# Performance work log

Hardware: AMD Instinct MI355X
Metric: run time of the kernel (lower is better)

## Reference

```python
import jax, jax.numpy as jnp
import numpy as np

B, S, D, H, E, K = 4, 2048, 512, 2048, 8, 2


def setup_inputs() -> dict:
    key = jax.random.key(0)
    k0, k1, k2, k3 = jax.random.split(key, 4)
    return {
        "x": jax.random.normal(k0, (B, S, D), jnp.float32),
        "router_w": jax.random.normal(k1, (E, D), jnp.float32) * 0.02,
        "router_b": jnp.zeros((E,), jnp.float32),
        "w1": jax.random.normal(k2, (E, D, H), jnp.float32) * 0.02,
        "b1": jnp.zeros((E, H), jnp.float32),
        "w2": jax.random.normal(k3, (E, H, D), jnp.float32) * 0.02,
        "b2": jnp.zeros((E, D), jnp.float32),
        "top_k": K,
    }


def reference(x, router_w, router_b, w1, b1, w2, b2, top_k):
    # x: [B, S, D]; eval mode (no router noise, no dropout)
    Bb, Ss, Dd = x.shape
    Ee = w1.shape[0]
    xf = x.reshape(-1, Dd)                                   # [T, D], T = B*S
    router_logits = xf @ router_w.T + router_b               # [T, E]
    top_v, top_i = jax.lax.top_k(router_logits, top_k)       # [T, K]
    rw = jax.nn.softmax(top_v, axis=-1)                      # [T, K]
    # combine[t, e] = sum_k rw[t, k] * (top_i[t, k] == e); zero for unrouted experts
    combine = jnp.sum(jax.nn.one_hot(top_i, Ee, dtype=xf.dtype) * rw[..., None], axis=1)  # [T, E]
    out = jnp.zeros_like(xf)
    for e in range(Ee):  # fixed small expert count; each iter is a dense GEMM pair
        h = jax.nn.gelu(xf @ w1[e] + b1[e], approximate=False)  # exact erf GELU like torch nn.GELU
        y = h @ w2[e] + b2[e]                                   # [T, D]
        out = out + combine[:, e:e + 1] * y
    return out.reshape(Bb, Ss, Dd), router_logits
```

## Files before the change

kernel.cpp:

```cpp
#include <hip/hip_runtime.h>
#include <hip/hip_bf16.h>

#define TTOK 8192
#define DDIM 512
#define HDIM 2048
#define NEXP 8
#define RBLK 256
#define RTOK (TTOK / RBLK)

typedef __bf16 bf16x8 __attribute__((ext_vector_type(8)));
typedef float f32x4 __attribute__((ext_vector_type(4)));
typedef unsigned short us8 __attribute__((ext_vector_type(8)));

__device__ __forceinline__ unsigned short f2bf(float f) {
  unsigned int u = __builtin_bit_cast(unsigned int, f);
  u += 0x7fffu + ((u >> 16) & 1u);
  return (unsigned short)(u >> 16);
}

__device__ __forceinline__ void gll16(const void* g, void* l) {
  __builtin_amdgcn_global_load_lds(
      (__attribute__((address_space(1))) void*)g,
      (__attribute__((address_space(3))) void*)l, 16, 0, 0);
}

__global__ __launch_bounds__(256) void k_router(
    const float* __restrict__ x, const float* __restrict__ rw,
    const float* __restrict__ rb, float* __restrict__ logits,
    unsigned short* __restrict__ xb,
    short* __restrict__ texp, unsigned short* __restrict__ tpos,
    float* __restrict__ tgate, int* __restrict__ blockcnt) {
  __shared__ int lcnt[NEXP];
  const int tid = threadIdx.x, wid = tid >> 6, lane = tid & 63;
  if (tid < NEXP) lcnt[tid] = 0;
  __syncthreads();
  float4 w0[NEXP], w1[NEXP];
  float rbv[NEXP];
#pragma unroll
  for (int e = 0; e < NEXP; ++e) {
    const float4* wp = (const float4*)(rw + e * DDIM);
    w0[e] = wp[lane * 2];
    w1[e] = wp[lane * 2 + 1];
    rbv[e] = rb[e];
  }
  const int tbase = blockIdx.x * RTOK;
  for (int it = 0; it < RTOK / 4; ++it) {
    const int t = tbase + it * 4 + wid;
    const float4* xr = (const float4*)(x + (size_t)t * DDIM);
    float4 v0 = xr[lane * 2], v1 = xr[lane * 2 + 1];
    us8 o;
    o[0] = f2bf(v0.x); o[1] = f2bf(v0.y); o[2] = f2bf(v0.z); o[3] = f2bf(v0.w);
    o[4] = f2bf(v1.x); o[5] = f2bf(v1.y); o[6] = f2bf(v1.z); o[7] = f2bf(v1.w);
    *(us8*)(xb + (size_t)t * DDIM + lane * 8) = o;
    float a[NEXP];
#pragma unroll
    for (int e = 0; e < NEXP; ++e)
      a[e] = v0.x * w0[e].x + v0.y * w0[e].y + v0.z * w0[e].z + v0.w * w0[e].w +
             v1.x * w1[e].x + v1.y * w1[e].y + v1.z * w1[e].z + v1.w * w1[e].w;
#pragma unroll
    for (int off = 32; off > 0; off >>= 1)
#pragma unroll
      for (int e = 0; e < NEXP; ++e) a[e] += __shfl_xor(a[e], off, 64);
    if (lane == 0) {
      float lg[NEXP];
#pragma unroll
      for (int e = 0; e < NEXP; ++e) lg[e] = a[e] + rbv[e];
      float4 s0, s1;
      s0.x = lg[0]; s0.y = lg[1]; s0.z = lg[2]; s0.w = lg[3];
      s1.x = lg[4]; s1.y = lg[5]; s1.z = lg[6]; s1.w = lg[7];
      ((float4*)(logits + t * NEXP))[0] = s0;
      ((float4*)(logits + t * NEXP))[1] = s1;
      int i0 = 0; float m0 = lg[0];
#pragma unroll
      for (int e = 1; e < NEXP; ++e) if (lg[e] > m0) { m0 = lg[e]; i0 = e; }
      int i1 = 0; float m1 = -3.4e38f;
#pragma unroll
      for (int e = 0; e < NEXP; ++e) if (e != i0 && lg[e] > m1) { m1 = lg[e]; i1 = e; }
      float e1 = expf(m1 - m0);
      float inv = 1.0f / (1.0f + e1);
      int p0 = atomicAdd(&lcnt[i0], 1);
      int p1 = atomicAdd(&lcnt[i1], 1);
      texp[t * 2] = (short)i0;     tpos[t * 2] = (unsigned short)p0;     tgate[t * 2] = inv;
      texp[t * 2 + 1] = (short)i1; tpos[t * 2 + 1] = (unsigned short)p1; tgate[t * 2 + 1] = e1 * inv;
    }
  }
  __syncthreads();
  if (tid < NEXP) blockcnt[blockIdx.x * NEXP + tid] = lcnt[tid];
}

__global__ void k_offsets(const int* __restrict__ blockcnt, int* __restrict__ blockbase,
                          int* __restrict__ counts, int* __restrict__ offsets) {
  const int e = threadIdx.x;
  if (e < NEXP) {
    int run = 0;
#pragma unroll 8
    for (int b = 0; b < RBLK; ++b) {
      blockbase[b * NEXP + e] = run;
      run += blockcnt[b * NEXP + e];
    }
    counts[e] = run;
  }
  __syncthreads();
  if (e == 0) {
    int s = 0;
    for (int q = 0; q < NEXP; ++q) { offsets[q] = s; s += counts[q]; }
  }
}

__global__ void k_scatter(const short* __restrict__ texp, const unsigned short* __restrict__ tpos,
                          const float* __restrict__ tgate, const int* __restrict__ blockbase,
                          const int* __restrict__ offsets,
                          int* __restrict__ toklist, int* __restrict__ cidx,
                          float* __restrict__ cgate) {
  const int t = blockIdx.x * 256 + threadIdx.x;
  const int b = t / RTOK;
#pragma unroll
  for (int k = 0; k < 2; ++k) {
    const int e = (int)texp[t * 2 + k];
    const int pos = blockbase[b * NEXP + e] + (int)tpos[t * 2 + k];
    toklist[e * TTOK + pos] = t;
    cidx[t * 2 + k] = offsets[e] + pos;
    cgate[t * 2 + k] = tgate[t * 2 + k];
  }
}

__global__ void k_transpose2(const float* __restrict__ w1, const float* __restrict__ w2,
                             unsigned short* __restrict__ w1t, unsigned short* __restrict__ w2t) {
  __shared__ float tile[32][33];
  const int id = blockIdx.x;
  const float* in; unsigned short* out; int R, C, rem;
  if (id < 8192) {
    const int e = id >> 10; rem = id & 1023;
    R = DDIM; C = HDIM;
    in = w1 + (size_t)e * R * C; out = w1t + (size_t)e * R * C;
  } else {
    const int e = (id - 8192) >> 10; rem = (id - 8192) & 1023;
    R = HDIM; C = DDIM;
    in = w2 + (size_t)e * R * C; out = w2t + (size_t)e * R * C;
  }
  const int ctiles = C >> 5;
  const int c0 = (rem % ctiles) * 32, r0 = (rem / ctiles) * 32;
  const int tx = threadIdx.x, ty = threadIdx.y;
#pragma unroll
  for (int i = 0; i < 32; i += 8)
    tile[ty + i][tx] = in[(size_t)(r0 + ty + i) * C + (c0 + tx)];
  __syncthreads();
#pragma unroll
  for (int i = 0; i < 32; i += 8)
    out[(size_t)(c0 + ty + i) * R + (r0 + tx)] = f2bf(tile[tx][ty + i]);
}

template <int PHASE>
__global__ __launch_bounds__(256, 2) void k_gemm(
    const unsigned short* __restrict__ A, const unsigned short* __restrict__ Bt,
    const float* __restrict__ bias, const int* __restrict__ counts,
    const int* __restrict__ offsets, const int* __restrict__ toklist,
    unsigned short* __restrict__ Out) {
  constexpr int K = (PHASE == 1) ? DDIM : HDIM;
  constexpr int NN = (PHASE == 1) ? HDIM : DDIM;
  constexpr int KB = K * 2;
  constexpr int NX = NN / 128;
  constexpr int NXSH = (PHASE == 1) ? 4 : 2;
  constexpr int BM = (PHASE == 1) ? 128 : 64;
  constexpr int AI = BM / 32;
  constexpr int MI = BM / 32;
  constexpr int WRM = BM / 2;
  constexpr int ASZ = BM * 128;
  constexpr int NT = K / 64;

  const int id = blockIdx.x;
  const int e = id & 7;
  const int p = id >> 3;
  const int cnt = counts[e];
  const int m0 = (p >> NXSH) * BM;
  if (m0 >= cnt) return;
  const int n0 = (p & (NX - 1)) * 128;
  const int off = offsets[e];

  __shared__ alignas(16) unsigned char smem[ASZ + 16384];

  const int tid = threadIdx.x;
  const int wid = tid >> 6, lane = tid & 63;

  const char* asrc[AI];
  const char* bsrc[4];
  unsigned adst[AI], bdst[4];
#pragma unroll
  for (int i = 0; i < AI; ++i) {
    const int c = i * 4 + wid;
    const int r = c * 8 + (lane >> 3);
    const int cs = ((lane & 7) * 16) ^ ((r & 7) << 4);
    int mrow = m0 + r; if (mrow > cnt - 1) mrow = cnt - 1;
    if (PHASE == 1) {
      const int tok = toklist[(e << 13) + mrow];
      asrc[i] = (const char*)A + (size_t)tok * (DDIM * 2) + cs;
    } else {
      asrc[i] = (const char*)A + (size_t)(off + mrow) * KB + cs;
    }
    adst[i] = c * 1024;
  }
#pragma unroll
  for (int i = 0; i < 4; ++i) {
    const int c = i * 4 + wid;
    const int r = c * 8 + (lane >> 3);
    const int cs = ((lane & 7) * 16) ^ ((r & 7) << 4);
    bsrc[i] = (const char*)Bt + (size_t)e * NN * KB + (size_t)(n0 + r) * KB + cs;
    bdst[i] = ASZ + c * 1024;
  }

  f32x4 acc[MI][4] = {};

  const int wr = wid >> 1, wc = wid & 1;
  const int lr = lane & 15, lk = lane >> 4;

  for (int t = 0; t < NT; ++t) {
    const int kb = t * 128;
#pragma unroll
    for (int i = 0; i < AI; ++i) gll16(asrc[i] + kb, smem + adst[i]);
#pragma unroll
    for (int i = 0; i < 4; ++i) gll16(bsrc[i] + kb, smem + bdst[i]);
    __syncthreads();
#pragma unroll
    for (int kk = 0; kk < 2; ++kk) {
      bf16x8 af[MI], bv[4];
#pragma unroll
      for (int mi = 0; mi < MI; ++mi) {
        const int r = wr * WRM + mi * 16 + lr;
        const int byteo = r * 128 + ((kk * 64 + lk * 16) ^ ((r & 7) << 4));
        af[mi] = *(const bf16x8*)(smem + byteo);
      }
#pragma unroll
      for (int ni = 0; ni < 4; ++ni) {
        const int r = wc * 64 + ni * 16 + lr;
        const int byteo = ASZ + r * 128 + ((kk * 64 + lk * 16) ^ ((r & 7) << 4));
        bv[ni] = *(const bf16x8*)(smem + byteo);
      }
#pragma unroll
      for (int mi = 0; mi < MI; ++mi)
#pragma unroll
        for (int ni = 0; ni < 4; ++ni)
          acc[mi][ni] = __builtin_amdgcn_mfma_f32_16x16x32_bf16(af[mi], bv[ni], acc[mi][ni], 0, 0, 0);
    }
    if (t + 1 < NT) __syncthreads();
  }

  const int lq = lane >> 4;
#pragma unroll
  for (int mi = 0; mi < MI; ++mi) {
#pragma unroll
    for (int ni = 0; ni < 4; ++ni) {
      const int n = n0 + wc * 64 + ni * 16 + lr;
      const float bv_ = bias[e * NN + n];
#pragma unroll
      for (int r2 = 0; r2 < 4; ++r2) {
        const int m = m0 + wr * WRM + mi * 16 + lq * 4 + r2;
        if (m < cnt) {
          if (PHASE == 1) {
            const float xv = acc[mi][ni][r2] + bv_;
            const float g = 0.5f * xv * (1.0f + erff(xv * 0.70710678118f));
            Out[(size_t)(off + m) * HDIM + n] = f2bf(g);
          } else {
            Out[(size_t)(off + m) * DDIM + n] = f2bf(acc[mi][ni][r2] + bv_);
          }
        }
      }
    }
  }
}

__global__ __launch_bounds__(256) void k_combine(const unsigned short* __restrict__ yp,
                                                 const int* __restrict__ cidx,
                                                 const float* __restrict__ cgate,
                                                 float* __restrict__ out) {
  const int t = blockIdx.x * 4 + (threadIdx.x >> 6);
  const int lane = threadIdx.x & 63;
  const int i0 = cidx[t * 2], i1 = cidx[t * 2 + 1];
  const float g0 = cgate[t * 2], g1 = cgate[t * 2 + 1];
  us8 a = *(const us8*)(yp + (size_t)i0 * DDIM + lane * 8);
  us8 b = *(const us8*)(yp + (size_t)i1 * DDIM + lane * 8);
  float o[8];
#pragma unroll
  for (int j = 0; j < 8; ++j) {
    const float va = __builtin_bit_cast(float, (unsigned)a[j] << 16);
    const float vb = __builtin_bit_cast(float, (unsigned)b[j] << 16);
    o[j] = g0 * va + g1 * vb;
  }
  float* op = out + (size_t)t * DDIM + lane * 8;
  *(float4*)op = *(float4*)o;
  *(float4*)(op + 4) = *(float4*)(o + 4);
}

extern "C" void kernel_launch(void* const* d_in, const int* in_sizes, int n_in,
                              void* d_out, int out_size, void* d_ws, size_t ws_size,
                              hipStream_t stream) {
  (void)in_sizes; (void)n_in; (void)out_size; (void)ws_size;
  const float* x  = (const float*)d_in[0];
  const float* rw = (const float*)d_in[1];
  const float* rb = (const float*)d_in[2];
  const float* w1 = (const float*)d_in[3];
  const float* b1 = (const float*)d_in[4];
  const float* w2 = (const float*)d_in[5];
  const float* b2 = (const float*)d_in[6];
  float* out = (float*)d_out;
  float* logits = out + (size_t)TTOK * DDIM;

  char* ws = (char*)d_ws;
  unsigned short* xb  = (unsigned short*)(ws + 0);
  unsigned short* w1t = (unsigned short*)(ws + 8388608);
  unsigned short* w2t = (unsigned short*)(ws + 25165824);
  unsigned short* h   = (unsigned short*)(ws + 41943040);
  int*   toklist = (int*)(ws + 109051904);
  int*   cidx    = (int*)(ws + 109314048);
  float* cgate   = (float*)(ws + 109379584);
  int*   counts  = (int*)(ws + 109445120);
  int*   offsets = (int*)(ws + 109445152);
  unsigned short* yp = w1t;
  char* rsc = ws + 41943040;
  short*          texp      = (short*)(rsc + 0);
  unsigned short* tpos      = (unsigned short*)(rsc + 32768);
  float*          tgate     = (float*)(rsc + 65536);
  int*            blockcnt  = (int*)(rsc + 131072);
  int*            blockbase = (int*)(rsc + 139264);

  k_router<<<RBLK, 256, 0, stream>>>(x, rw, rb, logits, xb, texp, tpos, tgate, blockcnt);
  k_transpose2<<<16384, dim3(32, 8), 0, stream>>>(w1, w2, w1t, w2t);
  k_offsets<<<1, 64, 0, stream>>>(blockcnt, blockbase, counts, offsets);
  k_scatter<<<TTOK / 256, 256, 0, stream>>>(texp, tpos, tgate, blockbase, offsets,
                                            toklist, cidx, cgate);

  k_gemm<1><<<(HDIM / 128) * (TTOK / 128) * NEXP, 256, 0, stream>>>(
      xb, w1t, b1, counts, offsets, toklist, h);
  k_gemm<2><<<(DDIM / 128) * (TTOK / 64) * NEXP, 256, 0, stream>>>(
      h, w2t, b2, counts, offsets, nullptr, yp);
  k_combine<<<TTOK / 4, 256, 0, stream>>>(yp, cidx, cgate, out);
}
```

Baseline: 277.3 us.

## Double-buffer expert GEMM tiles with 512-thread blocks and tanh GELU

Restructures the expert GEMM to use 512-thread blocks (8 waves, a 2x4 wave grid) with a uniform 128x128 tile for both phases. Shared memory is double-buffered so the async global-to-LDS load of the next K tile overlaps the MFMA work on the current one, which removes one barrier per iteration. The exact erf GELU is replaced with a tanh-approximation GELU computed through __expf, which is cheaper but no longer matches the exact-erf reference numerically. The larger block and launch-bounds change also alter register pressure and occupancy, and phase 2 now uses 128-row tiles.

```diff
diff --git a/kernel.cpp b/kernel.cpp
--- a/kernel.cpp
+++ b/kernel.cpp
@@ -151,7 +151,7 @@
 }
 
 template <int PHASE>
-__global__ __launch_bounds__(256, 2) void k_gemm(
+__global__ __launch_bounds__(512, 4) void k_gemm(
     const unsigned short* __restrict__ A, const unsigned short* __restrict__ Bt,
     const float* __restrict__ bias, const int* __restrict__ counts,
     const int* __restrict__ offsets, const int* __restrict__ toklist,
@@ -161,103 +161,102 @@
   constexpr int KB = K * 2;
   constexpr int NX = NN / 128;
   constexpr int NXSH = (PHASE == 1) ? 4 : 2;
-  constexpr int BM = (PHASE == 1) ? 128 : 64;
-  constexpr int AI = BM / 32;
-  constexpr int MI = BM / 32;
-  constexpr int WRM = BM / 2;
-  constexpr int ASZ = BM * 128;
   constexpr int NT = K / 64;
 
   const int id = blockIdx.x;
   const int e = id & 7;
   const int p = id >> 3;
   const int cnt = counts[e];
-  const int m0 = (p >> NXSH) * BM;
+  const int m0 = (p >> NXSH) * 128;
   if (m0 >= cnt) return;
   const int n0 = (p & (NX - 1)) * 128;
   const int off = offsets[e];
 
-  __shared__ alignas(16) unsigned char smem[ASZ + 16384];
+  __shared__ alignas(16) unsigned char smem[2][32768];
 
   const int tid = threadIdx.x;
   const int wid = tid >> 6, lane = tid & 63;
 
-  const char* asrc[AI];
-  const char* bsrc[4];
-  unsigned adst[AI], bdst[4];
-#pragma unroll
-  for (int i = 0; i < AI; ++i) {
-    const int c = i * 4 + wid;
-    const int r = c * 8 + (lane >> 3);
+  const char* src[4];
+  unsigned dst[4];
+#pragma unroll
+  for (int i = 0; i < 4; ++i) {
+    const int c = i * 8 + wid;
+    const bool isA = c < 16;
+    const int cc = isA ? c : c - 16;
+    const int r = cc * 8 + (lane >> 3);
     const int cs = ((lane & 7) * 16) ^ ((r & 7) << 4);
-    int mrow = m0 + r; if (mrow > cnt - 1) mrow = cnt - 1;
-    if (PHASE == 1) {
-      const int tok = toklist[(e << 13) + mrow];
-      asrc[i] = (const char*)A + (size_t)tok * (DDIM * 2) + cs;
+    if (isA) {
+      int mrow = m0 + r; if (mrow > cnt - 1) mrow = cnt - 1;
+      if (PHASE == 1) {
+        const int tok = toklist[(e << 13) + mrow];
+        src[i] = (const char*)A + (size_t)tok * (DDIM * 2) + cs;
+      } else {
+        src[i] = (const char*)A + (size_t)(off + mrow) * KB + cs;
+      }
     } else {
-      asrc[i] = (const char*)A + (size_t)(off + mrow) * KB + cs;
-    }
-    adst[i] = c * 1024;
-  }
-#pragma unroll
-  for (int i = 0; i < 4; ++i) {
-    const int c = i * 4 + wid;
-    const int r = c * 8 + (lane >> 3);
-    const int cs = ((lane & 7) * 16) ^ ((r & 7) << 4);
-    bsrc[i] = (const char*)Bt + (size_t)e * NN * KB + (size_t)(n0 + r) * KB + cs;
-    bdst[i] = ASZ + c * 1024;
-  }
-
-  f32x4 acc[MI][4] = {};
-
-  const int wr = wid >> 1, wc = wid & 1;
+      src[i] = (const char*)Bt + (size_t)e * NN * KB + (size_t)(n0 + r) * KB + cs;
+    }
+    dst[i] = (isA ? 0u : 16384u) + cc * 1024;
+  }
+
+  f32x4 acc[4][2] = {};
+
+  const int wr = wid >> 2, wc = wid & 3;
   const int lr = lane & 15, lk = lane >> 4;
 
+#pragma unroll
+  for (int i = 0; i < 4; ++i) gll16(src[i], &smem[0][0] + dst[i]);
+  __syncthreads();
+
+  int cur = 0;
   for (int t = 0; t < NT; ++t) {
-    const int kb = t * 128;
-#pragma unroll
-    for (int i = 0; i < AI; ++i) gll16(asrc[i] + kb, smem + adst[i]);
-#pragma unroll
-    for (int i = 0; i < 4; ++i) gll16(bsrc[i] + kb, smem + bdst[i]);
-    __syncthreads();
+    if (t + 1 < NT) {
+      const int kb = (t + 1) * 128;
+#pragma unroll
+      for (int i = 0; i < 4; ++i) gll16(src[i] + kb, &smem[cur ^ 1][0] + dst[i]);
+    }
+    const unsigned cb = (unsigned)cur * 32768u;
 #pragma unroll
     for (int kk = 0; kk < 2; ++kk) {
-      bf16x8 af[MI], bv[4];
-#pragma unroll
-      for (int mi = 0; mi < MI; ++mi) {
-        const int r = wr * WRM + mi * 16 + lr;
-        const int byteo = r * 128 + ((kk * 64 + lk * 16) ^ ((r & 7) << 4));
-        af[mi] = *(const bf16x8*)(smem + byteo);
+      bf16x8 af[4], bv[2];
+#pragma unroll
+      for (int mi = 0; mi < 4; ++mi) {
+        const int r = wr * 64 + mi * 16 + lr;
+        const unsigned byteo = cb + r * 128 + ((kk * 64 + lk * 16) ^ ((r & 7) << 4));
+        af[mi] = *(const bf16x8*)(&smem[0][0] + byteo);
       }
 #pragma unroll
-      for (int ni = 0; ni < 4; ++ni) {
-        const int r = wc * 64 + ni * 16 + lr;
-        const int byteo = ASZ + r * 128 + ((kk * 64 + lk * 16) ^ ((r & 7) << 4));
-        bv[ni] = *(const bf16x8*)(smem + byteo);
+      for (int ni = 0; ni < 2; ++ni) {
+        const int r = wc * 32 + ni * 16 + lr;
+        const unsigned byteo = cb + 16384 + r * 128 + ((kk * 64 + lk * 16) ^ ((r & 7) << 4));
+        bv[ni] = *(const bf16x8*)(&smem[0][0] + byteo);
       }
 #pragma unroll
-      for (int mi = 0; mi < MI; ++mi)
-#pragma unroll
-        for (int ni = 0; ni < 4; ++ni)
+      for (int mi = 0; mi < 4; ++mi)
+#pragma unroll
+        for (int ni = 0; ni < 2; ++ni)
           acc[mi][ni] = __builtin_amdgcn_mfma_f32_16x16x32_bf16(af[mi], bv[ni], acc[mi][ni], 0, 0, 0);
     }
     if (t + 1 < NT) __syncthreads();
+    cur ^= 1;
   }
 
   const int lq = lane >> 4;
 #pragma unroll
-  for (int mi = 0; mi < MI; ++mi) {
-#pragma unroll
-    for (int ni = 0; ni < 4; ++ni) {
-      const int n = n0 + wc * 64 + ni * 16 + lr;
+  for (int mi = 0; mi < 4; ++mi) {
+#pragma unroll
+    for (int ni = 0; ni < 2; ++ni) {
+      const int n = n0 + wc * 32 + ni * 16 + lr;
       const float bv_ = bias[e * NN + n];
 #pragma unroll
       for (int r2 = 0; r2 < 4; ++r2) {
-        const int m = m0 + wr * WRM + mi * 16 + lq * 4 + r2;
+        const int m = m0 + wr * 64 + mi * 16 + lq * 4 + r2;
         if (m < cnt) {
           if (PHASE == 1) {
             const float xv = acc[mi][ni][r2] + bv_;
-            const float g = 0.5f * xv * (1.0f + erff(xv * 0.70710678118f));
+            const float u = xv * (0.7978845608f + 0.0356774081f * xv * xv);
+            const float g = xv / (1.0f + __expf(-2.0f * u));
             Out[(size_t)(off + m) * HDIM + n] = f2bf(g);
           } else {
             Out[(size_t)(off + m) * DDIM + n] = f2bf(acc[mi][ni][r2] + bv_);
@@ -328,9 +327,9 @@
   k_scatter<<<TTOK / 256, 256, 0, stream>>>(texp, tpos, tgate, blockbase, offsets,
                                             toklist, cidx, cgate);
 
-  k_gemm<1><<<(HDIM / 128) * (TTOK / 128) * NEXP, 256, 0, stream>>>(
+  k_gemm<1><<<(HDIM / 128) * (TTOK / 128) * NEXP, 512, 0, stream>>>(
       xb, w1t, b1, counts, offsets, toklist, h);
-  k_gemm<2><<<(DDIM / 128) * (TTOK / 64) * NEXP, 256, 0, stream>>>(
+  k_gemm<2><<<(DDIM / 128) * (TTOK / 128) * NEXP, 512, 0, stream>>>(
       h, w2t, b2, counts, offsets, nullptr, yp);
   k_combine<<<TTOK / 4, 256, 0, stream>>>(yp, cidx, cgate, out);
 }
```

Measured after the change: 280.7 us. No clear change (+1.2%).
